# Optimization experiments

Measured on AMD Instinct MI355X. Metric: run time of the kernel, lower is better.

## Reference

```python
import jax, jax.numpy as jnp
import numpy as np

A = -0.75  # torch bicubic coefficient

def _cc1(x):
    return ((A + 2.0) * x - (A + 3.0)) * x * x + 1.0

def _cc2(x):
    return ((A * x - 5.0 * A) * x + 8.0 * A) * x - 4.0 * A

def cubic_weights(t):
    # t in [0,1); returns [4, ...] weights for taps at offsets -1,0,1,2
    return jnp.stack([_cc2(t + 1.0), _cc1(t), _cc1(1.0 - t), _cc2(2.0 - t)], axis=0)

def resize_matrix(l_in, l_out):
    # dense [l_out, l_in] bicubic (align_corners=True) interpolation matrix
    i = jnp.arange(l_out, dtype=jnp.float32)
    src = i * (l_in - 1) / (l_out - 1)
    i0 = jnp.floor(src)
    t = src - i0
    w = cubic_weights(t)  # [4, l_out]
    i0 = i0.astype(jnp.int32)
    rows = jnp.arange(l_out)
    M = jnp.zeros((l_out, l_in), dtype=jnp.float32)
    for k in range(4):
        idx = jnp.clip(i0 - 1 + k, 0, l_in - 1)  # border replicate (torch upsample)
        M = M.at[rows, idx].add(w[k])
    return M

def create_grid(H, W):
    # channel 0: x-coordinate (varies along W), channel 1: y-coordinate (varies along H)
    gx = jnp.broadcast_to(jnp.linspace(-1.0, 1.0, W, dtype=jnp.float32)[None, :], (H, W))
    gy = jnp.broadcast_to(jnp.linspace(-1.0, 1.0, H, dtype=jnp.float32)[:, None], (H, W))
    return jnp.stack([gx, gy], axis=0)  # [2, H, W]

def grid_sample_bicubic(inp, grid):
    # inp [B,C,H,W], grid [B,Ho,Wo,2] normalized coords, align_corners=True, zeros padding
    B, C, H, W = inp.shape
    x = (grid[..., 0] + 1.0) * 0.5 * (W - 1)
    y = (grid[..., 1] + 1.0) * 0.5 * (H - 1)
    ixf = jnp.floor(x)
    iyf = jnp.floor(y)
    wx = cubic_weights(x - ixf)  # [4,B,Ho,Wo]
    wy = cubic_weights(y - iyf)
    ix = ixf.astype(jnp.int32)
    iy = iyf.astype(jnp.int32)
    inp_flat = inp.reshape(B, C, H * W)
    gather = jax.vmap(lambda f, i: f[:, i])  # ([C,HW],[Ho,Wo]) -> [C,Ho,Wo]
    out = jnp.zeros((B, C) + grid.shape[1:3], dtype=inp.dtype)
    for m in range(4):
        yy = iy - 1 + m
        yv = (yy >= 0) & (yy < H)
        yc = jnp.clip(yy, 0, H - 1)
        for n in range(4):
            xx = ix - 1 + n
            valid = yv & (xx >= 0) & (xx < W)
            xc = jnp.clip(xx, 0, W - 1)
            lin = yc * W + xc  # [B,Ho,Wo]
            vals = gather(inp_flat, lin)  # [B,C,Ho,Wo]
            w = jnp.where(valid, wy[m] * wx[n], 0.0)[:, None, :, :]
            out = out + vals * w
    return out

def setup_inputs() -> dict:
    key = jax.random.key(0)
    k1, k2 = jax.random.split(key)
    inp = jax.random.normal(k1, (8, 32, 256, 256), dtype=jnp.float32)
    flow = jax.random.normal(k2, (8, 2, 64, 64), dtype=jnp.float32)
    return {"input": inp, "flow": flow}

def reference(input, flow):
    H, W = 256, 256
    p = int(max(H, W) * 0.1)  # 25
    Hp, Wp = H + 2 * p, W + 2 * p
    # replication pad input
    inp_p = jnp.pad(input, ((0, 0), (0, 0), (p, p), (p, p)), mode='edge')
    # bicubic upsample flow to (H,W), align_corners=True
    Mh = resize_matrix(flow.shape[2], H)
    Mw = resize_matrix(flow.shape[3], W)
    flow_r = jnp.einsum('Hh,bchw,Ww->bcHW', Mh, flow, Mw)
    grid = create_grid(H, W)
    f = flow_r - grid[None]
    f = jnp.pad(f, ((0, 0), (0, 0), (p, p), (p, p)))  # constant zero pad
    f = f + create_grid(Hp, Wp)[None]
    flow_grid = jnp.transpose(f, (0, 2, 3, 1))  # [B,Hp,Wp,2]
    out = grid_sample_bicubic(inp_p, flow_grid)
    return out[:, :, p:-p, p:-p]
```

## Files before the change

kernel.cpp:

```cpp
#include <hip/hip_runtime.h>
#include <hip/hip_fp16.h>

__device__ __forceinline__ float cc1(float x) {
    return (1.25f * x - 2.25f) * x * x + 1.0f;
}
__device__ __forceinline__ float cc2(float x) {
    return ((-0.75f * x + 3.75f) * x - 6.0f) * x + 3.0f;
}

__device__ __forceinline__ void axis64(int o, float w[4], int idx[4]) {
    float src = (float)o * 63.0f / 255.0f;
    float f = floorf(src);
    float t = src - f;
    w[0] = cc2(t + 1.0f);
    w[1] = cc1(t);
    w[2] = cc1(1.0f - t);
    w[3] = cc2(2.0f - t);
    int i0 = (int)f;
#pragma unroll
    for (int k = 0; k < 4; ++k) idx[k] = min(max(i0 - 1 + k, 0), 63);
}

__device__ __forceinline__ bool pixel_taps(const float* __restrict__ flow, int b,
                                           int i, int j,
                                           float wx[4], float wy[4],
                                           int xs[4], int ys[4]) {
    float wwy[4], wwx[4];
    int yi4[4], xi4[4];
    axis64(i, wwy, yi4);
    axis64(j, wwx, xi4);

    const float* fb = flow + (long)b * 2 * 4096;
    float fx = 0.f, fy = 0.f;
#pragma unroll
    for (int m = 0; m < 4; ++m) {
        const float* r0 = fb + yi4[m] * 64;
        float sx = 0.f, sy = 0.f;
#pragma unroll
        for (int n = 0; n < 4; ++n) {
            sx += wwx[n] * r0[xi4[n]];
            sy += wwx[n] * r0[4096 + xi4[n]];
        }
        fx += wwy[m] * sx;
        fy += wwy[m] * sy;
    }

    const float gx256 = -1.0f + 2.0f * (float)j / 255.0f;
    const float gy256 = -1.0f + 2.0f * (float)i / 255.0f;
    const float gx306 = -1.0f + 2.0f * (float)(j + 25) / 305.0f;
    const float gy306 = -1.0f + 2.0f * (float)(i + 25) / 305.0f;
    const float x = (fx - gx256 + gx306 + 1.0f) * 152.5f;
    const float y = (fy - gy256 + gy306 + 1.0f) * 152.5f;

    const float ixf = floorf(x), iyf = floorf(y);
    const float tx = x - ixf, ty = y - iyf;
    wx[0] = cc2(tx + 1.f); wx[1] = cc1(tx); wx[2] = cc1(1.f - tx); wx[3] = cc2(2.f - tx);
    wy[0] = cc2(ty + 1.f); wy[1] = cc1(ty); wy[2] = cc1(1.f - ty); wy[3] = cc2(2.f - ty);
    const int ix = (int)ixf, iy = (int)iyf;

    bool anyx = false, anyy = false;
#pragma unroll
    for (int n = 0; n < 4; ++n) {
        int xx = ix - 1 + n;
        bool vx = (xx >= 0) && (xx < 306);
        anyx |= vx;
        if (!vx) wx[n] = 0.f;
        xs[n] = min(max(xx - 25, 0), 255);

        int yy = iy - 1 + n;
        bool vy = (yy >= 0) && (yy < 306);
        anyy |= vy;
        if (!vy) wy[n] = 0.f;
        ys[n] = min(max(yy - 25, 0), 255);
    }
    return anyx && anyy;
}

__global__ __launch_bounds__(256) void transpose_clast_h_kernel(
    const float* __restrict__ inp, __half* __restrict__ ws)
{
    __shared__ float lds[32 * 260];
    const int blk = blockIdx.x;
    const int b = blk & 7;
    const int p0 = (blk >> 3) << 8;
    const float* ib = inp + ((long)b << 21);
    const int tid = threadIdx.x;
    const int l = tid & 63;
    const int w = tid >> 6;

#pragma unroll
    for (int k = 0; k < 8; ++k) {
        const int c = (k << 2) + w;
        const float4 v = *(const float4*)(ib + ((long)c << 16) + p0 + (l << 2));
        *(float4*)&lds[c * 260 + (l << 2)] = v;
    }
    __syncthreads();

    __half* wsb = ws + (((long)b << 16) + p0) * 32;
#pragma unroll
    for (int q = 0; q < 4; ++q) {
        const int f  = (q << 8) + tid;
        const int px = f >> 2;
        const int c0 = (f & 3) << 3;
        __half2 h[4];
#pragma unroll
        for (int i = 0; i < 4; ++i) {
            float a  = lds[(c0 + 2 * i + 0) * 260 + px];
            float bb = lds[(c0 + 2 * i + 1) * 260 + px];
            h[i] = __float22half2_rn(make_float2(a, bb));
        }
        *(float4*)(wsb + ((long)f << 3)) = *(float4*)h;
    }
}

__global__ __launch_bounds__(256, 4) void gather_clast_h_kernel(
    const __half* __restrict__ ws,
    const float* __restrict__ flow,
    float* __restrict__ out,
    int toff)
{
    __shared__ float w_lds[16][64];
    __shared__ int   o_lds[16][64];
    __shared__ int   v_lds[64];

    const int tid = threadIdx.x;
    const int blk = blockIdx.x;
    const int b = blk & 7;
    const int pidx0 = ((blk >> 3) + toff) << 6;

    if (tid < 64) {
        const int pidx = pidx0 + tid;
        const int i = pidx >> 8, j = pidx & 255;
        float wx[4], wy[4];
        int xs[4], ys[4];
        const bool valid = pixel_taps(flow, b, i, j, wx, wy, xs, ys);
        v_lds[tid] = valid ? 1 : 0;
#pragma unroll
        for (int m = 0; m < 4; ++m)
#pragma unroll
            for (int n = 0; n < 4; ++n) {
                w_lds[m * 4 + n][tid] = wy[m] * wx[n];
                o_lds[m * 4 + n][tid] = (ys[m] << 13) + (xs[n] << 5);
            }
    }
    __syncthreads();

    const int lane = tid & 63;
    const int wv   = tid >> 6;
    const int pl   = (wv << 4) + (lane & 15);
    const int g    = lane >> 4;

    const __half* baseh = ws + ((long)b << 21) + (g << 3);

    float acc[8];
#pragma unroll
    for (int k = 0; k < 8; ++k) acc[k] = 0.f;

    if (v_lds[pl]) {
        float4 v[16];
#pragma unroll
        for (int k = 0; k < 16; ++k)
            v[k] = *(const float4*)(baseh + o_lds[k][pl]);

#pragma unroll
        for (int k = 0; k < 16; ++k) {
            const float w = w_lds[k][pl];
            const __half2* h = (const __half2*)&v[k];
#pragma unroll
            for (int m = 0; m < 4; ++m) {
                float2 f = __half22float2(h[m]);
                acc[2 * m + 0] += w * f.x;
                acc[2 * m + 1] += w * f.y;
            }
        }
    }

    const int pidx = pidx0 + pl;
    float* op = out + ((long)b << 21) + ((long)(g << 3) << 16) + pidx;
#pragma unroll
    for (int k = 0; k < 8; ++k)
        op[(long)k << 16] = acc[k];
}

__global__ __launch_bounds__(256) void warp_bicubic_fallback(
    const float* __restrict__ inp,
    const float* __restrict__ flow,
    float* __restrict__ out)
{
    const int j = threadIdx.x;
    const int i = blockIdx.x & 255;
    const int b = blockIdx.x >> 8;

    float wx[4], wy[4];
    int xs[4], ys[4];
    pixel_taps(flow, b, i, j, wx, wy, xs, ys);

    float* op = out + (long)b * 32 * 65536 + i * 256 + j;
    const float* ib = inp + (long)b * 32 * 65536;
#pragma unroll 2
    for (int c = 0; c < 32; ++c) {
        const float* s = ib + c * 65536;
        float acc = 0.f;
#pragma unroll
        for (int m = 0; m < 4; ++m) {
            float wm = wy[m];
            if (wm != 0.f) {
                const float* r = s + ys[m] * 256;
                acc += wm * (wx[0] * r[xs[0]] + wx[1] * r[xs[1]] +
                             wx[2] * r[xs[2]] + wx[3] * r[xs[3]]);
            }
        }
        op[c * 65536] = acc;
    }
}

extern "C" void kernel_launch(void* const* d_in, const int* in_sizes, int n_in,
                              void* d_out, int out_size, void* d_ws, size_t ws_size,
                              hipStream_t stream) {
    const float* inp  = (const float*)d_in[0];
    const float* flow = (const float*)d_in[1];
    float* out = (float*)d_out;

    const size_t need = (size_t)8 * 32 * 256 * 256 * sizeof(__half);
    if (ws_size >= need) {
        __half* ws = (__half*)d_ws;
        transpose_clast_h_kernel<<<dim3(2048), dim3(256), 0, stream>>>(inp, ws);
        gather_clast_h_kernel<<<dim3(4096), dim3(256), 0, stream>>>(ws, flow, out, 0);
        gather_clast_h_kernel<<<dim3(4096), dim3(256), 0, stream>>>(ws, flow, out, 512);
    } else {
        warp_bicubic_fallback<<<dim3(8 * 256), dim3(256), 0, stream>>>(inp, flow, out);
    }
}
```

Measured before the change: 156.7 us.

## Split bicubic taps across waves per pixel and reduce partials in LDS

The gather kernel now handles 16 pixels per block instead of 64. Each wave takes one tap row (4 taps), and the four row partials are summed through shared memory before the store. This raises memory-level parallelism per pixel and cuts register pressure from 16 float4 loads per thread to 4. The two launches are merged into a single grid of 32768 blocks. The cost is an extra LDS reduction and barrier, only a quarter of the threads doing the final stores, and eight times as many blocks, each paying for the tap setup.

Measured after the change: 166.1 us. +6.0%, slower.

```diff
diff --git a/kernel.cpp b/kernel.cpp
--- a/kernel.cpp
+++ b/kernel.cpp
@@ -113,22 +113,22 @@
     }
 }
 
-__global__ __launch_bounds__(256, 4) void gather_clast_h_kernel(
+__global__ __launch_bounds__(256) void gather_clast_h_kernel(
     const __half* __restrict__ ws,
     const float* __restrict__ flow,
-    float* __restrict__ out,
-    int toff)
+    float* __restrict__ out)
 {
-    __shared__ float w_lds[16][64];
-    __shared__ int   o_lds[16][64];
-    __shared__ int   v_lds[64];
+    __shared__ float w_lds[16][16];
+    __shared__ int   o_lds[16][16];
+    __shared__ int   v_lds[16];
+    __shared__ float p_lds[4][4][8][16];
 
     const int tid = threadIdx.x;
     const int blk = blockIdx.x;
     const int b = blk & 7;
-    const int pidx0 = ((blk >> 3) + toff) << 6;
-
-    if (tid < 64) {
+    const int pidx0 = (blk >> 3) << 4;
+
+    if (tid < 16) {
         const int pidx = pidx0 + tid;
         const int i = pidx >> 8, j = pidx & 255;
         float wx[4], wy[4];
@@ -145,41 +145,54 @@
     }
     __syncthreads();
 
-    const int lane = tid & 63;
-    const int wv   = tid >> 6;
-    const int pl   = (wv << 4) + (lane & 15);
-    const int g    = lane >> 4;
-
-    const __half* baseh = ws + ((long)b << 21) + (g << 3);
+    const int m  = tid >> 6;
+    const int g  = tid & 3;
+    const int px = (tid >> 2) & 15;
 
     float acc[8];
 #pragma unroll
     for (int k = 0; k < 8; ++k) acc[k] = 0.f;
 
-    if (v_lds[pl]) {
-        float4 v[16];
-#pragma unroll
-        for (int k = 0; k < 16; ++k)
-            v[k] = *(const float4*)(baseh + o_lds[k][pl]);
-
-#pragma unroll
-        for (int k = 0; k < 16; ++k) {
-            const float w = w_lds[k][pl];
-            const __half2* h = (const __half2*)&v[k];
-#pragma unroll
-            for (int m = 0; m < 4; ++m) {
-                float2 f = __half22float2(h[m]);
-                acc[2 * m + 0] += w * f.x;
-                acc[2 * m + 1] += w * f.y;
+    if (v_lds[px]) {
+        const __half* baseh = ws + ((long)b << 21) + (g << 3);
+        float wr[4];
+        float4 v[4];
+#pragma unroll
+        for (int n = 0; n < 4; ++n) wr[n] = w_lds[m * 4 + n][px];
+#pragma unroll
+        for (int n = 0; n < 4; ++n)
+            v[n] = *(const float4*)(baseh + o_lds[m * 4 + n][px]);
+#pragma unroll
+        for (int n = 0; n < 4; ++n) {
+            const __half2* h = (const __half2*)&v[n];
+            const float w = wr[n];
+#pragma unroll
+            for (int q = 0; q < 4; ++q) {
+                float2 f = __half22float2(h[q]);
+                acc[2 * q + 0] += w * f.x;
+                acc[2 * q + 1] += w * f.y;
             }
         }
     }
 
-    const int pidx = pidx0 + pl;
-    float* op = out + ((long)b << 21) + ((long)(g << 3) << 16) + pidx;
-#pragma unroll
-    for (int k = 0; k < 8; ++k)
-        op[(long)k << 16] = acc[k];
+#pragma unroll
+    for (int k = 0; k < 8; ++k) p_lds[m][g][k][px] = acc[k];
+    __syncthreads();
+
+    if (tid < 64) {
+        const int g2  = tid & 3;
+        const int px2 = tid >> 2;
+        float o8[8];
+#pragma unroll
+        for (int k = 0; k < 8; ++k)
+            o8[k] = p_lds[0][g2][k][px2] + p_lds[1][g2][k][px2] +
+                    p_lds[2][g2][k][px2] + p_lds[3][g2][k][px2];
+        const int pidx = pidx0 + px2;
+        float* op = out + ((long)b << 21) + ((long)(g2 << 3) << 16) + pidx;
+#pragma unroll
+        for (int k = 0; k < 8; ++k)
+            op[(long)k << 16] = o8[k];
+    }
 }
 
 __global__ __launch_bounds__(256) void warp_bicubic_fallback(
@@ -225,8 +238,7 @@
     if (ws_size >= need) {
         __half* ws = (__half*)d_ws;
         transpose_clast_h_kernel<<<dim3(2048), dim3(256), 0, stream>>>(inp, ws);
-        gather_clast_h_kernel<<<dim3(4096), dim3(256), 0, stream>>>(ws, flow, out, 0);
-        gather_clast_h_kernel<<<dim3(4096), dim3(256), 0, stream>>>(ws, flow, out, 512);
+        gather_clast_h_kernel<<<dim3(32768), dim3(256), 0, stream>>>(ws, flow, out);
     } else {
         warp_bicubic_fallback<<<dim3(8 * 256), dim3(256), 0, stream>>>(inp, flow, out);
     }
```
